# Optimization experiments

Measured on AMD Instinct MI355X. Metric: run time of the kernel, lower is better.

## Reference

```python
import jax, jax.numpy as jnp
import numpy as np

B, S, IN, OUT = 4, 32, 8192, 8192


def setup_inputs() -> dict:
    key = jax.random.key(0)
    k1, k2, k3, k4 = jax.random.split(key, 4)
    x = jax.random.normal(k1, (B, S, IN), dtype=jnp.float32)
    # FP8-e4m3 stored weight: round-trip through fp8 so values are representable,
    # then keep as fp32 (the module upcasts to fp32 before the matmul anyway).
    w = jax.random.normal(k2, (OUT, IN), dtype=jnp.float32)
    weight = w.astype(jnp.float8_e4m3fn).astype(jnp.float32)
    # per-output-channel scale, strictly positive small values
    weight_scale = jax.random.uniform(k3, (OUT, 1), dtype=jnp.float32,
                                      minval=1e-3, maxval=2e-2)
    bias = (jax.random.normal(k4, (OUT,), dtype=jnp.float32) * 0.01).astype(jnp.float16)
    return {"x": x, "weight": weight, "weight_scale": weight_scale, "bias": bias}


def reference(x, weight, weight_scale, bias):
    # dequantize fp8 weight to fp32 with per-channel scale  [OUT, IN]
    dq_w = weight * weight_scale
    # x @ dq_w.T  -> [B, S, OUT]
    out = jnp.einsum("bsi,oi->bso", x.astype(jnp.float32), dq_w)
    out = out + bias.astype(jnp.float32)
    return out
```

## Files before the change

kernel.cpp:

```cpp
#include <hip/hip_runtime.h>
#include <hip/hip_bf16.h>
#include <hip/hip_fp16.h>


namespace {
constexpr int MM = 128;
constexpr int NN = 8192;
constexpr int KK = 8192;
constexpr int KSPLIT = 8;
constexpr int KPB = KK / KSPLIT;
constexpr int KT = 128;
constexpr int NIT = KPB / KT;
constexpr int LDSW = KT + 8;

constexpr size_t WS_SCALE_OFF = 0;
constexpr size_t WS_BIAS_OFF  = 8192 * 4;
constexpr size_t WS_XSW_OFF   = 65536;
constexpr size_t WS_NEED      = WS_XSW_OFF + (size_t)MM * KK * 2;

typedef __attribute__((ext_vector_type(8))) short bf16x8;
typedef __attribute__((ext_vector_type(4))) float f32x4;
}

__global__ __launch_bounds__(256)
void cfp8_prep(const float* __restrict__ x,
               const float* __restrict__ c1, const float* __restrict__ c2,
               unsigned char* __restrict__ ws)
{
    const int bid = blockIdx.x;
    const int tid = threadIdx.x;

    if (bid < 32) {
        __shared__ int s_c1s, s_kind;
        if (tid < 64) {
            float v = c1[tid * 64];
            unsigned long long b = __ballot((v > 1e-4f) && (v < 0.5f));
            int c1s = (b == ~0ull) ? 1 : 0;
            const void* bp = c1s ? (const void*)c2 : (const void*)c1;
            float vf = __half2float(((const __half*)bp)[tid * 64]);
            unsigned long long bf_ = __ballot((vf < 0.5f) && (vf > -0.5f));
            float vb = __bfloat162float(((const __hip_bfloat16*)bp)[tid * 64]);
            unsigned long long bb = __ballot((vb < 0.5f) && (vb > -0.5f));
            if (tid == 0) {
                s_c1s  = c1s;
                s_kind = (bf_ == ~0ull) ? 0 : ((bb == ~0ull) ? 1 : 2);
            }
        }
        __syncthreads();
        const float* scalep = s_c1s ? c1 : c2;
        const void*  biasp  = s_c1s ? (const void*)c2 : (const void*)c1;
        const int i = bid * 256 + tid;
        float bsv;
        if (s_kind == 0)      bsv = __half2float(((const __half*)biasp)[i]);
        else if (s_kind == 1) bsv = __bfloat162float(((const __hip_bfloat16*)biasp)[i]);
        else                  bsv = ((const float*)biasp)[i];
        ((float*)(ws + WS_SCALE_OFF))[i] = scalep[i];
        ((float*)(ws + WS_BIAS_OFF))[i]  = bsv;
    } else {
        const int g = (bid - 32) * 256 + tid;
        const float4* src = (const float4*)x + (size_t)g * 2;
        float4 a = src[0], b = src[1];
        const int m  = g >> 10;
        const int kg = g & 1023;
        const int s  = kg >> 2;
        const int r8 = kg & 3;
        const int t  = m >> 4;
        const int lm = m & 15;
        const int l  = r8 * 16 + lm;
        union { __hip_bfloat16 h[8]; uint4 u; } p;
        p.h[0] = __float2bfloat16(a.x); p.h[1] = __float2bfloat16(a.y);
        p.h[2] = __float2bfloat16(a.z); p.h[3] = __float2bfloat16(a.w);
        p.h[4] = __float2bfloat16(b.x); p.h[5] = __float2bfloat16(b.y);
        p.h[6] = __float2bfloat16(b.z); p.h[7] = __float2bfloat16(b.w);
        ((uint4*)(ws + WS_XSW_OFF))[(size_t)(s * 8 + t) * 64 + l] = p.u;
    }
}

__global__ __launch_bounds__(256, 4)
void cfp8_gemm(const float* __restrict__ w, const unsigned char* __restrict__ ws,
               float* __restrict__ out)
{
    __shared__ __align__(16) __hip_bfloat16 lw[4][2][16 * LDSW];

    const int tid  = threadIdx.x;
    const int lane = tid & 63;
    const int wid  = tid >> 6;
    const int kz   = blockIdx.y;
    const int n0   = blockIdx.x * 64 + wid * 16;
    const size_t kbase = (size_t)kz * KPB;

    const __hip_bfloat16* xsw = (const __hip_bfloat16*)(ws + WS_XSW_OFF);
    const float* wsc = (const float*)(ws + WS_SCALE_OFF);
    const float* wbs = (const float*)(ws + WS_BIAS_OFF);

    const int l16  = lane & 15;
    const int quad = lane >> 4;

    const float sc = wsc[n0 + l16];
    const float bs = (kz == 0) ? wbs[n0 + l16] : 0.0f;

    const int srow = lane >> 5;
    const int scol = (lane & 31) * 4;
    const float* wg = w + (size_t)(n0 + srow) * KK + kbase + scol;

    float4 wf[8];
#pragma unroll
    for (int i = 0; i < 8; ++i)
        wf[i] = *(const float4*)(wg + (size_t)(2 * i) * KK);

    f32x4 acc[8];
#pragma unroll
    for (int t = 0; t < 8; ++t) acc[t] = (f32x4){0.f, 0.f, 0.f, 0.f};

    for (int kt = 0; kt < NIT; ++kt) {
        __hip_bfloat16* lb = &lw[wid][kt & 1][0];

#pragma unroll
        for (int i = 0; i < 8; ++i) {
            union { __hip_bfloat16 h[4]; uint2 u; } p;
            p.h[0] = __float2bfloat16(wf[i].x);
            p.h[1] = __float2bfloat16(wf[i].y);
            p.h[2] = __float2bfloat16(wf[i].z);
            p.h[3] = __float2bfloat16(wf[i].w);
            *(uint2*)&lb[(2 * i + srow) * LDSW + scol] = p.u;
        }

        if (kt + 1 < NIT) {
            const float* wgn = wg + (size_t)(kt + 1) * KT;
#pragma unroll
            for (int i = 0; i < 8; ++i)
                wf[i] = *(const float4*)(wgn + (size_t)(2 * i) * KK);
        }

        const int sgl0 = kz * 32 + kt * 4;
#pragma unroll
        for (int ss = 0; ss < 4; ++ss) {
            bf16x8 bfrag = *(const bf16x8*)&lb[l16 * LDSW + ss * 32 + quad * 8];
            const uint4* xp = (const uint4*)xsw + (size_t)(sgl0 + ss) * 8 * 64 + lane;
            bf16x8 af[8];
#pragma unroll
            for (int t = 0; t < 8; ++t) {
                uint4 u = xp[(size_t)t * 64];
                af[t] = *(bf16x8*)&u;
            }
#pragma unroll
            for (int t = 0; t < 8; ++t)
                acc[t] = __builtin_amdgcn_mfma_f32_16x16x32_bf16(
                    af[t], bfrag, acc[t], 0, 0, 0);
        }
    }

#pragma unroll
    for (int t = 0; t < 8; ++t) {
#pragma unroll
        for (int r = 0; r < 4; ++r) {
            atomicAdd(out + (size_t)(t * 16 + quad * 4 + r) * NN + n0 + l16,
                      acc[t][r] * sc + bs);
        }
    }
}

namespace fb {
constexpr int NT = 64;
constexpr int KTf = 32;
constexpr int NITf = KPB / KTf;
constexpr int LDSP = KTf + 8;
}

__global__ __launch_bounds__(256, 4)
void cfp8lin_mfma2(const float* __restrict__ x, const float* __restrict__ w,
                   const float* __restrict__ c1, const float* __restrict__ c2,
                   float* __restrict__ out)
{
    using namespace fb;
    __shared__ __align__(16) __hip_bfloat16 lx[2][MM * LDSP];
    __shared__ __align__(16) __hip_bfloat16 lw[2][NT * LDSP];
    __shared__ float s_scale[NT];
    __shared__ float s_bias[NT];
    __shared__ int s_c1_is_scale;
    __shared__ int s_bias_kind;

    const int tid = threadIdx.x;
    const int n0 = blockIdx.x * NT;
    const int kz = blockIdx.y;
    const size_t kbase = (size_t)kz * KPB;

    if (tid < 64) {
        float v = c1[tid * 64];
        unsigned long long b = __ballot((v > 1e-4f) && (v < 0.5f));
        int c1s = (b == ~0ull) ? 1 : 0;
        const void* bp = c1s ? (const void*)c2 : (const void*)c1;
        float vf = __half2float(((const __half*)bp)[tid * 64]);
        unsigned long long bf_ = __ballot((vf < 0.5f) && (vf > -0.5f));
        float vb = __bfloat162float(((const __hip_bfloat16*)bp)[tid * 64]);
        unsigned long long bb = __ballot((vb < 0.5f) && (vb > -0.5f));
        if (tid == 0) {
            s_c1_is_scale = c1s;
            s_bias_kind = (bf_ == ~0ull) ? 0 : ((bb == ~0ull) ? 1 : 2);
        }
    }

    const int lrow = tid >> 3;
    const int lc4  = tid & 7;
    const float* xg = x + (size_t)lrow * KK + kbase + lc4 * 4;
    const float* wg = w + (size_t)(n0 + lrow) * KK + kbase + lc4 * 4;

    float4 xv[4], wv[2];
    auto load_tile = [&](int kt) {
        const size_t ko = (size_t)kt * KTf;
#pragma unroll
        for (int i = 0; i < 4; ++i)
            xv[i] = *(const float4*)(xg + (size_t)(i * 32) * KK + ko);
#pragma unroll
        for (int i = 0; i < 2; ++i)
            wv[i] = *(const float4*)(wg + (size_t)(i * 32) * KK + ko);
    };
    load_tile(0);

    const int lane = tid & 63;
    const int wid  = tid >> 6;
    const int wm0  = wid * 32;
    const int l16  = lane & 15;
    const int quad = lane >> 4;
    const int kcol = quad * 8;

    f32x4 acc[2][4];
#pragma unroll
    for (int i = 0; i < 2; ++i)
#pragma unroll
        for (int j = 0; j < 4; ++j) acc[i][j] = (f32x4){0.f, 0.f, 0.f, 0.f};

    for (int kt = 0; kt < NITf; ++kt) {
        const int buf = kt & 1;
#pragma unroll
        for (int i = 0; i < 4; ++i) {
            union { __hip_bfloat16 b[4]; uint2 u; } p;
            p.b[0] = __float2bfloat16(xv[i].x); p.b[1] = __float2bfloat16(xv[i].y);
            p.b[2] = __float2bfloat16(xv[i].z); p.b[3] = __float2bfloat16(xv[i].w);
            *(uint2*)&lx[buf][(i * 32 + lrow) * LDSP + lc4 * 4] = p.u;
        }
#pragma unroll
        for (int i = 0; i < 2; ++i) {
            union { __hip_bfloat16 b[4]; uint2 u; } p;
            p.b[0] = __float2bfloat16(wv[i].x); p.b[1] = __float2bfloat16(wv[i].y);
            p.b[2] = __float2bfloat16(wv[i].z); p.b[3] = __float2bfloat16(wv[i].w);
            *(uint2*)&lw[buf][(i * 32 + lrow) * LDSP + lc4 * 4] = p.u;
        }
        load_tile((kt + 1 < NITf) ? (kt + 1) : 0);
        __syncthreads();
        bf16x8 af[2], bw[4];
#pragma unroll
        for (int i = 0; i < 2; ++i)
            af[i] = *(const bf16x8*)&lx[buf][(wm0 + i * 16 + l16) * LDSP + kcol];
#pragma unroll
        for (int j = 0; j < 4; ++j)
            bw[j] = *(const bf16x8*)&lw[buf][(j * 16 + l16) * LDSP + kcol];
#pragma unroll
        for (int i = 0; i < 2; ++i)
#pragma unroll
            for (int j = 0; j < 4; ++j)
                acc[i][j] = __builtin_amdgcn_mfma_f32_16x16x32_bf16(
                    af[i], bw[j], acc[i][j], 0, 0, 0);
    }

    __syncthreads();
    const float* scalep = s_c1_is_scale ? c1 : c2;
    const void*  biasp  = s_c1_is_scale ? (const void*)c2 : (const void*)c1;
    if (tid < fb::NT) {
        s_scale[tid] = scalep[n0 + tid];
        float b = 0.0f;
        if (kz == 0) {
            if (s_bias_kind == 0)      b = __half2float(((const __half*)biasp)[n0 + tid]);
            else if (s_bias_kind == 1) b = __bfloat162float(((const __hip_bfloat16*)biasp)[n0 + tid]);
            else                       b = ((const float*)biasp)[n0 + tid];
        }
        s_bias[tid] = b;
    }
    __syncthreads();

#pragma unroll
    for (int j = 0; j < 4; ++j) {
        const int nl = j * 16 + l16;
        const float scv = s_scale[nl];
        const float bsv = s_bias[nl];
#pragma unroll
        for (int i = 0; i < 2; ++i) {
            const int mb = wm0 + i * 16 + quad * 4;
#pragma unroll
            for (int r = 0; r < 4; ++r)
                atomicAdd(out + (size_t)(mb + r) * NN + n0 + nl,
                          acc[i][j][r] * scv + bsv);
        }
    }
}

extern "C" void kernel_launch(void* const* d_in, const int* in_sizes, int n_in,
                              void* d_out, int out_size, void* d_ws, size_t ws_size,
                              hipStream_t stream) {
    int iw = 0;
    for (int i = 1; i < n_in; ++i) if (in_sizes[i] > in_sizes[iw]) iw = i;
    int ix = -1;
    for (int i = 0; i < n_in; ++i)
        if (i != iw && (ix < 0 || in_sizes[i] > in_sizes[ix])) ix = i;
    const float* c1 = nullptr;
    const float* c2 = nullptr;
    for (int i = 0; i < n_in; ++i) {
        if (i == iw || i == ix) continue;
        if (!c1) c1 = (const float*)d_in[i];
        else     c2 = (const float*)d_in[i];
    }
    const float* w = (const float*)d_in[iw];
    const float* x = (const float*)d_in[ix];
    float* out = (float*)d_out;

    hipMemsetAsync(d_out, 0, (size_t)out_size * sizeof(float), stream);

    if (ws_size >= WS_NEED && d_ws != nullptr) {
        unsigned char* ws = (unsigned char*)d_ws;
        cfp8_prep<<<dim3(32 + 512), dim3(256), 0, stream>>>(x, c1, c2, ws);
        cfp8_gemm<<<dim3(NN / 64, KSPLIT), dim3(256), 0, stream>>>(w, ws, out);
    } else {
        dim3 grid(NN / fb::NT, KSPLIT);
        cfp8lin_mfma2<<<grid, dim3(256), 0, stream>>>(x, w, c1, c2, out);
    }
}
```

Measured before the change: 418.4 us.

## Load weights directly into MFMA fragments, dropping LDS staging, with 2x2 warp tiling

The GEMM kernel stops staging converted weight tiles through shared memory. Each lane now loads its own fp32 weight fragment from global memory, converts it to bf16 in registers and feeds it straight to the MFMA. Warps are rearranged into a 2x2 grid of 64 rows by 32 columns, so each x fragment is reused across two weight column tiles, with register double-buffering of both operands. This removes the LDS writes and reads and the associated latency. The cost is strided 32-byte weight loads per lane that may coalesce less well than the old 512-byte row loads.

Result: slower. 445.4 us (+6.5%).

```diff
diff --git a/kernel.cpp b/kernel.cpp
--- a/kernel.cpp
+++ b/kernel.cpp
@@ -9,9 +9,7 @@
 constexpr int KK = 8192;
 constexpr int KSPLIT = 8;
 constexpr int KPB = KK / KSPLIT;
-constexpr int KT = 128;
-constexpr int NIT = KPB / KT;
-constexpr int LDSW = KT + 8;
+constexpr int NSS = KPB / 32;
 
 constexpr size_t WS_SCALE_OFF = 0;
 constexpr size_t WS_BIAS_OFF  = 8192 * 4;
@@ -77,85 +75,102 @@
 }
 
 __global__ __launch_bounds__(256, 4)
-void cfp8_gemm(const float* __restrict__ w, const unsigned char* __restrict__ ws,
-               float* __restrict__ out)
+void cfp8_gemm2(const float* __restrict__ w, const unsigned char* __restrict__ ws,
+                float* __restrict__ out)
 {
-    __shared__ __align__(16) __hip_bfloat16 lw[4][2][16 * LDSW];
-
     const int tid  = threadIdx.x;
     const int lane = tid & 63;
     const int wid  = tid >> 6;
+    const int nsub = wid & 1;
+    const int msub = wid >> 1;
     const int kz   = blockIdx.y;
-    const int n0   = blockIdx.x * 64 + wid * 16;
+    const int n0w  = blockIdx.x * 64 + nsub * 32;
     const size_t kbase = (size_t)kz * KPB;
 
-    const __hip_bfloat16* xsw = (const __hip_bfloat16*)(ws + WS_XSW_OFF);
-    const float* wsc = (const float*)(ws + WS_SCALE_OFF);
-    const float* wbs = (const float*)(ws + WS_BIAS_OFF);
+    const uint4* xsw4 = (const uint4*)(ws + WS_XSW_OFF);
+    const float* wsc  = (const float*)(ws + WS_SCALE_OFF);
+    const float* wbs  = (const float*)(ws + WS_BIAS_OFF);
 
     const int l16  = lane & 15;
     const int quad = lane >> 4;
 
-    const float sc = wsc[n0 + l16];
-    const float bs = (kz == 0) ? wbs[n0 + l16] : 0.0f;
-
-    const int srow = lane >> 5;
-    const int scol = (lane & 31) * 4;
-    const float* wg = w + (size_t)(n0 + srow) * KK + kbase + scol;
-
-    float4 wf[8];
-#pragma unroll
-    for (int i = 0; i < 8; ++i)
-        wf[i] = *(const float4*)(wg + (size_t)(2 * i) * KK);
-
-    f32x4 acc[8];
-#pragma unroll
-    for (int t = 0; t < 8; ++t) acc[t] = (f32x4){0.f, 0.f, 0.f, 0.f};
-
-    for (int kt = 0; kt < NIT; ++kt) {
-        __hip_bfloat16* lb = &lw[wid][kt & 1][0];
-
-#pragma unroll
-        for (int i = 0; i < 8; ++i) {
-            union { __hip_bfloat16 h[4]; uint2 u; } p;
-            p.h[0] = __float2bfloat16(wf[i].x);
-            p.h[1] = __float2bfloat16(wf[i].y);
-            p.h[2] = __float2bfloat16(wf[i].z);
-            p.h[3] = __float2bfloat16(wf[i].w);
-            *(uint2*)&lb[(2 * i + srow) * LDSW + scol] = p.u;
-        }
-
-        if (kt + 1 < NIT) {
-            const float* wgn = wg + (size_t)(kt + 1) * KT;
-#pragma unroll
-            for (int i = 0; i < 8; ++i)
-                wf[i] = *(const float4*)(wgn + (size_t)(2 * i) * KK);
-        }
-
-        const int sgl0 = kz * 32 + kt * 4;
-#pragma unroll
-        for (int ss = 0; ss < 4; ++ss) {
-            bf16x8 bfrag = *(const bf16x8*)&lb[l16 * LDSW + ss * 32 + quad * 8];
-            const uint4* xp = (const uint4*)xsw + (size_t)(sgl0 + ss) * 8 * 64 + lane;
-            bf16x8 af[8];
-#pragma unroll
-            for (int t = 0; t < 8; ++t) {
-                uint4 u = xp[(size_t)t * 64];
-                af[t] = *(bf16x8*)&u;
-            }
-#pragma unroll
-            for (int t = 0; t < 8; ++t)
-                acc[t] = __builtin_amdgcn_mfma_f32_16x16x32_bf16(
-                    af[t], bfrag, acc[t], 0, 0, 0);
-        }
-    }
-
-#pragma unroll
-    for (int t = 0; t < 8; ++t) {
+    const float sc0 = wsc[n0w + l16];
+    const float sc1 = wsc[n0w + 16 + l16];
+    const float bs0 = (kz == 0) ? wbs[n0w + l16] : 0.0f;
+    const float bs1 = (kz == 0) ? wbs[n0w + 16 + l16] : 0.0f;
+
+    const float* wr0 = w + (size_t)(n0w + l16) * KK + kbase + quad * 8;
+    const float* wr1 = wr0 + (size_t)16 * KK;
+
+    const int sg0 = kz * NSS;
+    const uint4* xb = xsw4 + (size_t)sg0 * 512 + (size_t)(msub * 4) * 64 + lane;
+
+    float4 wfb[2][2][2];
+    uint4  afb[2][4];
+
+#define LOAD_B(buf, s)                                                   \
+    do {                                                                 \
+        wfb[buf][0][0] = *(const float4*)(wr0 + (s) * 32);               \
+        wfb[buf][0][1] = *(const float4*)(wr0 + (s) * 32 + 4);           \
+        wfb[buf][1][0] = *(const float4*)(wr1 + (s) * 32);               \
+        wfb[buf][1][1] = *(const float4*)(wr1 + (s) * 32 + 4);           \
+    } while (0)
+#define LOAD_A(buf, s)                                                   \
+    do {                                                                 \
+        const uint4* xp = xb + (size_t)(s) * 512;                        \
+        afb[buf][0] = xp[0];                                             \
+        afb[buf][1] = xp[64];                                            \
+        afb[buf][2] = xp[128];                                           \
+        afb[buf][3] = xp[192];                                           \
+    } while (0)
+
+    LOAD_B(0, 0);
+    LOAD_A(0, 0);
+
+    f32x4 acc[4][2];
+#pragma unroll
+    for (int t = 0; t < 4; ++t) {
+        acc[t][0] = (f32x4){0.f, 0.f, 0.f, 0.f};
+        acc[t][1] = (f32x4){0.f, 0.f, 0.f, 0.f};
+    }
+
+#pragma unroll 2
+    for (int s = 0; s < NSS; ++s) {
+        const int buf = s & 1;
+        const int nxt = buf ^ 1;
+        const int sn = (s + 1 < NSS) ? (s + 1) : 0;
+
+        LOAD_B(nxt, sn);
+        LOAD_A(nxt, sn);
+
+        bf16x8 bw[2];
+#pragma unroll
+        for (int j = 0; j < 2; ++j) {
+            union { __hip_bfloat16 h[8]; bf16x8 v; } p;
+            const float* f = (const float*)&wfb[buf][j][0];
+#pragma unroll
+            for (int i = 0; i < 8; ++i) p.h[i] = __float2bfloat16(f[i]);
+            bw[j] = p.v;
+        }
+
+#pragma unroll
+        for (int t = 0; t < 4; ++t) {
+            bf16x8 af = *(bf16x8*)&afb[buf][t];
+            acc[t][0] = __builtin_amdgcn_mfma_f32_16x16x32_bf16(af, bw[0], acc[t][0], 0, 0, 0);
+            acc[t][1] = __builtin_amdgcn_mfma_f32_16x16x32_bf16(af, bw[1], acc[t][1], 0, 0, 0);
+        }
+    }
+#undef LOAD_A
+#undef LOAD_B
+
+#pragma unroll
+    for (int t = 0; t < 4; ++t) {
+        const int mb = msub * 64 + t * 16 + quad * 4;
 #pragma unroll
         for (int r = 0; r < 4; ++r) {
-            atomicAdd(out + (size_t)(t * 16 + quad * 4 + r) * NN + n0 + l16,
-                      acc[t][r] * sc + bs);
+            float* o = out + (size_t)(mb + r) * NN + n0w;
+            atomicAdd(o + l16,      acc[t][0][r] * sc0 + bs0);
+            atomicAdd(o + 16 + l16, acc[t][1][r] * sc1 + bs1);
         }
     }
 }
@@ -318,7 +333,7 @@
     if (ws_size >= WS_NEED && d_ws != nullptr) {
         unsigned char* ws = (unsigned char*)d_ws;
         cfp8_prep<<<dim3(32 + 512), dim3(256), 0, stream>>>(x, c1, c2, ws);
-        cfp8_gemm<<<dim3(NN / 64, KSPLIT), dim3(256), 0, stream>>>(w, ws, out);
+        cfp8_gemm2<<<dim3(NN / 64, KSPLIT), dim3(256), 0, stream>>>(w, ws, out);
     } else {
         dim3 grid(NN / fb::NT, KSPLIT);
         cfp8lin_mfma2<<<grid, dim3(256), 0, stream>>>(x, w, c1, c2, out);
```

## Use register-direct 128x128 GEMM tiles with split-K partials and a reduce kernel

Applied to the files above, without the earlier changes.

The split-K GEMM is rewritten so each wave computes a 64x64 output tile with a 4x4 grid of MFMAs. Weights are loaded straight from global memory into registers in B-fragment layout, removing the per-wave LDS staging buffer. Atomic accumulation into the memset output is replaced by per-split partial buffers in the workspace, which a separate reduce kernel sums and adds bias to. This raises operand reuse and drops atomics, but needs a much larger workspace and adds the write and read of the partials. It also loses the explicit register prefetch of the next weight tile.

Measured after the change: 426.3 us. Within noise of the previous version (+1.9%).

```diff
diff --git a/kernel.cpp b/kernel.cpp
--- a/kernel.cpp
+++ b/kernel.cpp
@@ -9,14 +9,13 @@
 constexpr int KK = 8192;
 constexpr int KSPLIT = 8;
 constexpr int KPB = KK / KSPLIT;
-constexpr int KT = 128;
-constexpr int NIT = KPB / KT;
-constexpr int LDSW = KT + 8;
+constexpr int NSS = KPB / 32;
 
 constexpr size_t WS_SCALE_OFF = 0;
 constexpr size_t WS_BIAS_OFF  = 8192 * 4;
 constexpr size_t WS_XSW_OFF   = 65536;
-constexpr size_t WS_NEED      = WS_XSW_OFF + (size_t)MM * KK * 2;
+constexpr size_t WS_PART_OFF  = WS_XSW_OFF + (size_t)MM * KK * 2;
+constexpr size_t WS_NEED      = WS_PART_OFF + (size_t)KSPLIT * MM * NN * 4;
 
 typedef __attribute__((ext_vector_type(8))) short bf16x8;
 typedef __attribute__((ext_vector_type(4))) float f32x4;
@@ -76,88 +75,96 @@
     }
 }
 
-__global__ __launch_bounds__(256, 4)
-void cfp8_gemm(const float* __restrict__ w, const unsigned char* __restrict__ ws,
-               float* __restrict__ out)
+__global__ __launch_bounds__(256, 2)
+void cfp8_gemm3(const float* __restrict__ w, unsigned char* __restrict__ ws)
 {
-    __shared__ __align__(16) __hip_bfloat16 lw[4][2][16 * LDSW];
-
     const int tid  = threadIdx.x;
     const int lane = tid & 63;
     const int wid  = tid >> 6;
+    const int wm0  = (wid & 1) * 64;
+    const int wn0  = (wid >> 1) * 64;
     const int kz   = blockIdx.y;
-    const int n0   = blockIdx.x * 64 + wid * 16;
+    const int n0   = blockIdx.x * 128;
     const size_t kbase = (size_t)kz * KPB;
 
-    const __hip_bfloat16* xsw = (const __hip_bfloat16*)(ws + WS_XSW_OFF);
-    const float* wsc = (const float*)(ws + WS_SCALE_OFF);
-    const float* wbs = (const float*)(ws + WS_BIAS_OFF);
+    const uint4* xsw4 = (const uint4*)(ws + WS_XSW_OFF);
+    const float* wsc  = (const float*)(ws + WS_SCALE_OFF);
 
     const int l16  = lane & 15;
     const int quad = lane >> 4;
 
-    const float sc = wsc[n0 + l16];
-    const float bs = (kz == 0) ? wbs[n0 + l16] : 0.0f;
-
-    const int srow = lane >> 5;
-    const int scol = (lane & 31) * 4;
-    const float* wg = w + (size_t)(n0 + srow) * KK + kbase + scol;
-
-    float4 wf[8];
-#pragma unroll
-    for (int i = 0; i < 8; ++i)
-        wf[i] = *(const float4*)(wg + (size_t)(2 * i) * KK);
-
-    f32x4 acc[8];
-#pragma unroll
-    for (int t = 0; t < 8; ++t) acc[t] = (f32x4){0.f, 0.f, 0.f, 0.f};
-
-    for (int kt = 0; kt < NIT; ++kt) {
-        __hip_bfloat16* lb = &lw[wid][kt & 1][0];
-
-#pragma unroll
-        for (int i = 0; i < 8; ++i) {
-            union { __hip_bfloat16 h[4]; uint2 u; } p;
-            p.h[0] = __float2bfloat16(wf[i].x);
-            p.h[1] = __float2bfloat16(wf[i].y);
-            p.h[2] = __float2bfloat16(wf[i].z);
-            p.h[3] = __float2bfloat16(wf[i].w);
-            *(uint2*)&lb[(2 * i + srow) * LDSW + scol] = p.u;
-        }
-
-        if (kt + 1 < NIT) {
-            const float* wgn = wg + (size_t)(kt + 1) * KT;
-#pragma unroll
-            for (int i = 0; i < 8; ++i)
-                wf[i] = *(const float4*)(wgn + (size_t)(2 * i) * KK);
-        }
-
-        const int sgl0 = kz * 32 + kt * 4;
-#pragma unroll
-        for (int ss = 0; ss < 4; ++ss) {
-            bf16x8 bfrag = *(const bf16x8*)&lb[l16 * LDSW + ss * 32 + quad * 8];
-            const uint4* xp = (const uint4*)xsw + (size_t)(sgl0 + ss) * 8 * 64 + lane;
-            bf16x8 af[8];
-#pragma unroll
-            for (int t = 0; t < 8; ++t) {
-                uint4 u = xp[(size_t)t * 64];
-                af[t] = *(bf16x8*)&u;
-            }
-#pragma unroll
-            for (int t = 0; t < 8; ++t)
-                acc[t] = __builtin_amdgcn_mfma_f32_16x16x32_bf16(
-                    af[t], bfrag, acc[t], 0, 0, 0);
-        }
-    }
-
-#pragma unroll
-    for (int t = 0; t < 8; ++t) {
-#pragma unroll
-        for (int r = 0; r < 4; ++r) {
-            atomicAdd(out + (size_t)(t * 16 + quad * 4 + r) * NN + n0 + l16,
-                      acc[t][r] * sc + bs);
-        }
-    }
+    const float* wr[4];
+#pragma unroll
+    for (int j = 0; j < 4; ++j)
+        wr[j] = w + (size_t)(n0 + wn0 + j * 16 + l16) * KK + kbase + quad * 8;
+
+    const uint4* xb = xsw4 + (size_t)(kz * NSS) * 512 + (size_t)(wm0 / 16) * 64 + lane;
+
+    f32x4 acc[4][4];
+#pragma unroll
+    for (int i = 0; i < 4; ++i)
+#pragma unroll
+        for (int j = 0; j < 4; ++j)
+            acc[i][j] = (f32x4){0.f, 0.f, 0.f, 0.f};
+
+    for (int ss = 0; ss < NSS; ++ss) {
+        const uint4* xp = xb + (size_t)ss * 512;
+        uint4 a0 = xp[0], a1 = xp[64], a2 = xp[128], a3 = xp[192];
+
+        bf16x8 bw[4];
+#pragma unroll
+        for (int j = 0; j < 4; ++j) {
+            float4 b0 = *(const float4*)(wr[j] + ss * 32);
+            float4 b1 = *(const float4*)(wr[j] + ss * 32 + 4);
+            union { __hip_bfloat16 h[8]; bf16x8 v; } p;
+            p.h[0] = __float2bfloat16(b0.x); p.h[1] = __float2bfloat16(b0.y);
+            p.h[2] = __float2bfloat16(b0.z); p.h[3] = __float2bfloat16(b0.w);
+            p.h[4] = __float2bfloat16(b1.x); p.h[5] = __float2bfloat16(b1.y);
+            p.h[6] = __float2bfloat16(b1.z); p.h[7] = __float2bfloat16(b1.w);
+            bw[j] = p.v;
+        }
+
+        bf16x8 af[4];
+        af[0] = *(bf16x8*)&a0; af[1] = *(bf16x8*)&a1;
+        af[2] = *(bf16x8*)&a2; af[3] = *(bf16x8*)&a3;
+
+#pragma unroll
+        for (int i = 0; i < 4; ++i)
+#pragma unroll
+            for (int j = 0; j < 4; ++j)
+                acc[i][j] = __builtin_amdgcn_mfma_f32_16x16x32_bf16(
+                    af[i], bw[j], acc[i][j], 0, 0, 0);
+    }
+
+    float* part = (float*)(ws + WS_PART_OFF) + (size_t)kz * MM * NN;
+#pragma unroll
+    for (int j = 0; j < 4; ++j) {
+        const int nl = wn0 + j * 16 + l16;
+        const float sc = wsc[n0 + nl];
+#pragma unroll
+        for (int i = 0; i < 4; ++i) {
+            const int mb = wm0 + i * 16 + quad * 4;
+#pragma unroll
+            for (int r = 0; r < 4; ++r)
+                part[(size_t)(mb + r) * NN + n0 + nl] = acc[i][j][r] * sc;
+        }
+    }
+}
+
+__global__ __launch_bounds__(256)
+void cfp8_reduce(const unsigned char* __restrict__ ws, float* __restrict__ out)
+{
+    const int e4 = blockIdx.x * 256 + threadIdx.x;
+    const float4* p = (const float4*)(ws + WS_PART_OFF);
+    float4 s = p[e4];
+#pragma unroll
+    for (int kz = 1; kz < KSPLIT; ++kz) {
+        float4 v = p[(size_t)kz * (MM * NN / 4) + e4];
+        s.x += v.x; s.y += v.y; s.z += v.z; s.w += v.w;
+    }
+    const float4 b = ((const float4*)(ws + WS_BIAS_OFF))[e4 & (NN / 4 - 1)];
+    s.x += b.x; s.y += b.y; s.z += b.z; s.w += b.w;
+    ((float4*)out)[e4] = s;
 }
 
 namespace fb {
@@ -313,13 +320,13 @@
     const float* x = (const float*)d_in[ix];
     float* out = (float*)d_out;
 
-    hipMemsetAsync(d_out, 0, (size_t)out_size * sizeof(float), stream);
-
     if (ws_size >= WS_NEED && d_ws != nullptr) {
         unsigned char* ws = (unsigned char*)d_ws;
         cfp8_prep<<<dim3(32 + 512), dim3(256), 0, stream>>>(x, c1, c2, ws);
-        cfp8_gemm<<<dim3(NN / 64, KSPLIT), dim3(256), 0, stream>>>(w, ws, out);
+        cfp8_gemm3<<<dim3(NN / 128, KSPLIT), dim3(256), 0, stream>>>(w, ws);
+        cfp8_reduce<<<dim3(MM * NN / 4 / 256), dim3(256), 0, stream>>>(ws, out);
     } else {
+        hipMemsetAsync(d_out, 0, (size_t)out_size * sizeof(float), stream);
         dim3 grid(NN / fb::NT, KSPLIT);
         cfp8lin_mfma2<<<grid, dim3(256), 0, stream>>>(x, w, c1, c2, out);
     }
```
